# Kernel tuning notes

Hardware: AMD Instinct MI355X
Metric: run time of the kernel (lower is better)

Reference implementation:

```python
import jax, jax.numpy as jnp
import numpy as np

K = 1024          # num_embeddings
D = 256           # embedding_dim
COMMIT = 0.1      # commitment_cost
EPS = float(np.finfo(np.float32).eps)


def setup_inputs() -> dict:
    key = jax.random.key(0)
    k1, k2 = jax.random.split(key)
    X = jax.random.normal(k1, (16, 4096, D), dtype=jnp.float32)
    # matches nn.Embedding init: uniform(-1/K, 1/K)
    emb_weight = jax.random.uniform(k2, (K, D), dtype=jnp.float32,
                                    minval=-1.0 / K, maxval=1.0 / K)
    return {"X": X, "emb_weight": emb_weight}


def reference(X, emb_weight):
    B, N, Dm = X.shape
    Xf = X.reshape(-1, Dm)                                  # [BN, D]
    dist = (jnp.sum(Xf * Xf, axis=-1, keepdims=True)
            + jnp.sum(emb_weight * emb_weight, axis=-1)
            - 2.0 * Xf @ emb_weight.T)                      # [BN, K]
    idx = jnp.argmin(dist, axis=-1)                         # [BN]
    # one-hot @ codebook == gather
    quantized = emb_weight[idx].reshape(X.shape)            # [B, N, D]
    # perplexity from one-hot mean == normalized counts
    counts = jnp.zeros((K,), dtype=X.dtype).at[idx].add(1.0)
    avg_probs = counts / Xf.shape[0]
    perplexity = jnp.exp(-jnp.sum(avg_probs * jnp.log(avg_probs + EPS)))
    # vq loss (learnable codebook branch)
    sg = jax.lax.stop_gradient
    e_latent = jnp.mean((sg(quantized) - X) ** 2)
    q_latent = jnp.mean((quantized - sg(X)) ** 2)
    loss_vq = q_latent + COMMIT * e_latent
    # straight-through estimator
    quantized_st = X + sg(quantized - X)
    encoding_indices = idx.reshape(B, N)
    return quantized_st, encoding_indices, perplexity, loss_vq
```

## Files before the change

### kernel.cpp

```cpp
#include <hip/hip_runtime.h>
#include <math.h>

#define ROWS 65536
#define DIM  256
#define KC   1024
#define NQ   (ROWS * DIM)


__device__ __forceinline__ float half_sq_sum(const float* __restrict__ a) {
    float4 u0 = *(const float4*)(a);
    float4 u1 = *(const float4*)(a + 4);
    float r0 = __fmul_rn(u0.x, u0.x);
    float r1 = __fmul_rn(u0.y, u0.y);
    float r2 = __fmul_rn(u0.z, u0.z);
    float r3 = __fmul_rn(u0.w, u0.w);
    float r4 = __fmul_rn(u1.x, u1.x);
    float r5 = __fmul_rn(u1.y, u1.y);
    float r6 = __fmul_rn(u1.z, u1.z);
    float r7 = __fmul_rn(u1.w, u1.w);
    for (int i = 8; i < 128; i += 8) {
        float4 v0 = *(const float4*)(a + i);
        float4 v1 = *(const float4*)(a + i + 4);
        r0 = __fadd_rn(r0, __fmul_rn(v0.x, v0.x));
        r1 = __fadd_rn(r1, __fmul_rn(v0.y, v0.y));
        r2 = __fadd_rn(r2, __fmul_rn(v0.z, v0.z));
        r3 = __fadd_rn(r3, __fmul_rn(v0.w, v0.w));
        r4 = __fadd_rn(r4, __fmul_rn(v1.x, v1.x));
        r5 = __fadd_rn(r5, __fmul_rn(v1.y, v1.y));
        r6 = __fadd_rn(r6, __fmul_rn(v1.z, v1.z));
        r7 = __fadd_rn(r7, __fmul_rn(v1.w, v1.w));
    }
    float s01 = __fadd_rn(r0, r1);
    float s23 = __fadd_rn(r2, r3);
    float s45 = __fadd_rn(r4, r5);
    float s67 = __fadd_rn(r6, r7);
    return __fadd_rn(__fadd_rn(s01, s23), __fadd_rn(s45, s67));
}

__device__ __forceinline__ float sq_sum_numpy(const float* __restrict__ p) {
    float h0 = half_sq_sum(p);
    float h1 = half_sq_sum(p + 128);
    return __fadd_rn(h0, h1);
}

__global__ __launch_bounds__(256) void k_prepB(const float* __restrict__ E,
                                               float* __restrict__ B32) {
    int j = blockIdx.x * 256 + threadIdx.x;
    if (j >= KC) return;
    B32[j] = sq_sum_numpy(E + (size_t)j * DIM);
}

#define TM 128
#define TN 128
#define TD 32
#define BUFF 4096
#define BSTR 8192

__global__ __launch_bounds__(256, 2) void k_pass1(
    const float* __restrict__ X, const float* __restrict__ E,
    const float* __restrict__ B32, int* __restrict__ idx32)
{
    __shared__ __align__(16) float sm[2 * BSTR];

    const int tid = threadIdx.x;
    const int tx  = tid & 15;
    const int ty  = tid >> 4;
    const int rowbase = blockIdx.x * TM;

    float4 xv0, xv1, xv2, xv3, ev0, ev1, ev2, ev3;

#define LOADR(cbn, dcn)                                                         \
    do {                                                                        \
        int fi_, r_, d4_;                                                       \
        fi_ = tid;       r_ = fi_ >> 3; d4_ = (fi_ & 7) << 2;                   \
        xv0 = *(const float4*)(X + (size_t)(rowbase + r_) * DIM + (dcn) + d4_); \
        ev0 = *(const float4*)(E + (size_t)((cbn) + r_) * DIM + (dcn) + d4_);   \
        fi_ = tid + 256; r_ = fi_ >> 3; d4_ = (fi_ & 7) << 2;                   \
        xv1 = *(const float4*)(X + (size_t)(rowbase + r_) * DIM + (dcn) + d4_); \
        ev1 = *(const float4*)(E + (size_t)((cbn) + r_) * DIM + (dcn) + d4_);   \
        fi_ = tid + 512; r_ = fi_ >> 3; d4_ = (fi_ & 7) << 2;                   \
        xv2 = *(const float4*)(X + (size_t)(rowbase + r_) * DIM + (dcn) + d4_); \
        ev2 = *(const float4*)(E + (size_t)((cbn) + r_) * DIM + (dcn) + d4_);   \
        fi_ = tid + 768; r_ = fi_ >> 3; d4_ = (fi_ & 7) << 2;                   \
        xv3 = *(const float4*)(X + (size_t)(rowbase + r_) * DIM + (dcn) + d4_); \
        ev3 = *(const float4*)(E + (size_t)((cbn) + r_) * DIM + (dcn) + d4_);   \
    } while (0)

#define WRITE1(Xs_, Es_, v_, e_, fif_)                                          \
    do {                                                                        \
        int r_ = (fif_) >> 3, d4_ = ((fif_) & 7) << 2;                          \
        int off_ = d4_ * 128 + ((((r_) >> 2) ^ (d4_ >> 2)) << 2) + ((r_) & 3);  \
        (Xs_)[off_]       = v_.x; (Xs_)[off_ + 128] = v_.y;                     \
        (Xs_)[off_ + 256] = v_.z; (Xs_)[off_ + 384] = v_.w;                     \
        (Es_)[off_]       = e_.x; (Es_)[off_ + 128] = e_.y;                     \
        (Es_)[off_ + 256] = e_.z; (Es_)[off_ + 384] = e_.w;                     \
    } while (0)

#define WRITEB(b)                                                               \
    do {                                                                        \
        float* Xs_ = sm + (b) * BSTR;                                           \
        float* Es_ = Xs_ + BUFF;                                                \
        WRITE1(Xs_, Es_, xv0, ev0, tid);                                        \
        WRITE1(Xs_, Es_, xv1, ev1, tid + 256);                                  \
        WRITE1(Xs_, Es_, xv2, ev2, tid + 512);                                  \
        WRITE1(Xs_, Es_, xv3, ev3, tid + 768);                                  \
    } while (0)

    LOADR(0, 0);

    {
        int r = tid >> 1, h = tid & 1;
        sm[(r << 1) + h] = half_sq_sum(X + (size_t)(rowbase + r) * DIM + (h << 7));
    }
    __syncthreads();
    float a8[8];
#pragma unroll
    for (int i = 0; i < 8; ++i)
        a8[i] = __fadd_rn(sm[(ty * 8 + i) * 2], sm[(ty * 8 + i) * 2 + 1]);
    __syncthreads();
    WRITEB(0);

    float v1[8]; int i1[8];
#pragma unroll
    for (int i = 0; i < 8; ++i) { v1[i] = 3.0e38f; i1[i] = 0; }

    int cur = 0;
    for (int cb8 = 0; cb8 < 8; ++cb8) {
        const int cbase = cb8 * TN;
        float4 bq0 = *(const float4*)(B32 + cbase + (tx << 2));
        float4 bq1 = *(const float4*)(B32 + cbase + 64 + (tx << 2));

        float acc[8][8];
#pragma unroll
        for (int i = 0; i < 8; ++i)
#pragma unroll
            for (int j = 0; j < 8; ++j) acc[i][j] = 0.0f;

        for (int dc8 = 0; dc8 < 8; ++dc8) {
            const int s = cb8 * 8 + dc8;
            __syncthreads();
            if (s < 63) {
                const int sn = s + 1;
                LOADR((sn >> 3) * TN, (sn & 7) * TD);
            }
            {
                const float* Xc = sm + cur * BSTR;
                const float* Ec = Xc + BUFF;
#pragma unroll 2
                for (int dq = 0; dq < 8; ++dq) {
                    const float* xp0 = Xc + dq * 512 + ((((ty << 1)    ) ^ dq) << 2);
                    const float* xp1 = Xc + dq * 512 + ((((ty << 1) | 1) ^ dq) << 2);
                    const float* ep0 = Ec + dq * 512 + ((tx ^ dq) << 2);
#pragma unroll
                    for (int ddi = 0; ddi < 4; ++ddi) {
                        float4 t0 = *(const float4*)(xp0 + ddi * 128);
                        float4 t1 = *(const float4*)(xp1 + ddi * 128);
                        float4 u0 = *(const float4*)(ep0 + ddi * 128);
                        float4 u1 = *(const float4*)(ep0 + ddi * 128 + 64);
                        float xr[8] = {t0.x, t0.y, t0.z, t0.w, t1.x, t1.y, t1.z, t1.w};
                        float er[8] = {u0.x, u0.y, u0.z, u0.w, u1.x, u1.y, u1.z, u1.w};
#pragma unroll
                        for (int i = 0; i < 8; ++i)
#pragma unroll
                            for (int j = 0; j < 8; ++j)
                                acc[i][j] = fmaf(xr[i], er[j], acc[i][j]);
                    }
                }
            }
            if (s < 63) WRITEB(cur ^ 1);
            cur ^= 1;
        }

        float bvv[8] = {bq0.x, bq0.y, bq0.z, bq0.w, bq1.x, bq1.y, bq1.z, bq1.w};
#pragma unroll
        for (int j = 0; j < 8; ++j) {
            const int c = cbase + ((j < 4) ? ((tx << 2) + j)
                                           : (64 + (tx << 2) + (j - 4)));
#pragma unroll
            for (int i = 0; i < 8; ++i) {
                float Cv  = __fmul_rn(2.0f, acc[i][j]);
                float t1v = __fadd_rn(a8[i], bvv[j]);
                float dv  = __fsub_rn(t1v, Cv);
                if (dv < v1[i]) { v1[i] = dv; i1[i] = c; }
            }
        }
    }

    __syncthreads();
    float* Mv = sm;
    int*   Mi = (int*)(sm + 2048);
#pragma unroll
    for (int i = 0; i < 8; ++i) {
        int r = ty * 8 + i;
        Mv[r * 16 + tx] = v1[i];
        Mi[r * 16 + tx] = i1[i];
    }
    __syncthreads();
    if (tid < TM) {
        int r = tid;
        float bv = Mv[r * 16];
        int   bi = Mi[r * 16];
        for (int t = 1; t < 16; ++t) {
            float av = Mv[r * 16 + t];
            int   ai = Mi[r * 16 + t];
            if (av < bv || (av == bv && ai < bi)) { bv = av; bi = ai; }
        }
        idx32[rowbase + r] = bi;
    }
#undef LOADR
#undef WRITE1
#undef WRITEB
}

__global__ __launch_bounds__(256) void k_out(
    const float* __restrict__ X, const float* __restrict__ E,
    const int* __restrict__ idx32, float* __restrict__ out0,
    double* __restrict__ lossacc)
{
    const int NF4 = NQ / 4;
    double s = 0.0;
    for (int g = blockIdx.x * blockDim.x + threadIdx.x; g < NF4;
         g += gridDim.x * blockDim.x) {
        int row = g >> 6;
        int d4  = g & 63;
        int j = idx32[row];
        float4 q = *(const float4*)(E + (size_t)j * DIM + d4 * 4);
        float4 x = *(const float4*)(X + (size_t)g * 4);
        *(float4*)(out0 + (size_t)g * 4) = q;
        double dx;
        dx = (double)q.x - (double)x.x; s = fma(dx, dx, s);
        dx = (double)q.y - (double)x.y; s = fma(dx, dx, s);
        dx = (double)q.z - (double)x.z; s = fma(dx, dx, s);
        dx = (double)q.w - (double)x.w; s = fma(dx, dx, s);
    }
#pragma unroll
    for (int off = 32; off > 0; off >>= 1) s += __shfl_down(s, off, 64);
    __shared__ double wsum[4];
    int lane = threadIdx.x & 63, wv = threadIdx.x >> 6;
    if (lane == 0) wsum[wv] = s;
    __syncthreads();
    if (threadIdx.x == 0) {
        double t = wsum[0] + wsum[1] + wsum[2] + wsum[3];
        atomicAdd(lossacc, t);
    }
}

__global__ __launch_bounds__(256) void k_idxout(
    const int* __restrict__ idx32, float* __restrict__ out1,
    int* __restrict__ counts)
{
    __shared__ int h[KC];
    for (int i = threadIdx.x; i < KC; i += 256) h[i] = 0;
    __syncthreads();
    int r = blockIdx.x * 256 + threadIdx.x;
    int j = idx32[r];
    out1[r] = (float)j;
    atomicAdd(&h[j], 1);
    __syncthreads();
    for (int i = threadIdx.x; i < KC; i += 256)
        if (h[i]) atomicAdd(&counts[i], h[i]);
}

__global__ void k_fin(const int* __restrict__ counts,
                      const double* __restrict__ lossacc,
                      float* __restrict__ out_pl)
{
    __shared__ double sh[256];
    double s = 0.0;
    for (int i = threadIdx.x; i < KC; i += 256) {
        double p = (double)counts[i] / 65536.0;
        s += p * log(p + 1.1920928955078125e-07);
    }
    sh[threadIdx.x] = s;
    __syncthreads();
    for (int off = 128; off > 0; off >>= 1) {
        if (threadIdx.x < off) sh[threadIdx.x] += sh[threadIdx.x + off];
        __syncthreads();
    }
    if (threadIdx.x == 0) {
        out_pl[0] = (float)exp(-sh[0]);
        out_pl[1] = (float)((*lossacc / (double)NQ) * 1.1);
    }
}

extern "C" void kernel_launch(void* const* d_in, const int* in_sizes, int n_in,
                              void* d_out, int out_size, void* d_ws, size_t ws_size,
                              hipStream_t stream) {
    const float* X = (const float*)d_in[0];
    const float* E = (const float*)d_in[1];
    float* out = (float*)d_out;
    char* ws = (char*)d_ws;

    double* lossacc = (double*)(ws + 0);
    int*    counts  = (int*)(ws + 16);
    float*  B32     = (float*)(ws + 4224);
    int*    idx32   = (int*)(ws + 270464);

    hipMemsetAsync(d_ws, 0, 4224, stream);

    hipLaunchKernelGGL(k_prepB, dim3(4),         dim3(256), 0, stream, E, B32);
    hipLaunchKernelGGL(k_pass1, dim3(ROWS / TM), dim3(256), 0, stream,
                       X, E, B32, idx32);
    hipLaunchKernelGGL(k_out,   dim3(2048),      dim3(256), 0, stream,
                       X, E, idx32, out, lossacc);
    hipLaunchKernelGGL(k_idxout, dim3(256),      dim3(256), 0, stream,
                       idx32, out + NQ, counts);
    hipLaunchKernelGGL(k_fin,   dim3(1),         dim3(256), 0, stream,
                       counts, lossacc, out + NQ + 65536);
}
```

Measured before the change: 571.1 us.

## Fuse gather, loss and histogram into distance kernel; halve depth tile for occupancy

```diff
diff --git a/kernel.cpp b/kernel.cpp
--- a/kernel.cpp
+++ b/kernel.cpp
@@ -52,44 +52,41 @@
 
 #define TM 128
 #define TN 128
-#define TD 32
-#define BUFF 4096
-#define BSTR 8192
-
-__global__ __launch_bounds__(256, 2) void k_pass1(
+#define TD 16
+#define BUFF 2048
+#define BSTR 4096
+
+__global__ __launch_bounds__(256, 4) void k_pass1(
     const float* __restrict__ X, const float* __restrict__ E,
-    const float* __restrict__ B32, int* __restrict__ idx32)
+    const float* __restrict__ B32, float* __restrict__ out0,
+    float* __restrict__ out1, int* __restrict__ counts,
+    double* __restrict__ lossacc)
 {
-    __shared__ __align__(16) float sm[2 * BSTR];
+    __shared__ __align__(16) float sm[2 * BSTR + 128];
+    float* asq = sm + 2 * BSTR;
 
     const int tid = threadIdx.x;
     const int tx  = tid & 15;
     const int ty  = tid >> 4;
     const int rowbase = blockIdx.x * TM;
 
-    float4 xv0, xv1, xv2, xv3, ev0, ev1, ev2, ev3;
+    float4 xv0, xv1, ev0, ev1;
 
 #define LOADR(cbn, dcn)                                                         \
     do {                                                                        \
         int fi_, r_, d4_;                                                       \
-        fi_ = tid;       r_ = fi_ >> 3; d4_ = (fi_ & 7) << 2;                   \
+        fi_ = tid;       r_ = fi_ >> 2; d4_ = (fi_ & 3) << 2;                   \
         xv0 = *(const float4*)(X + (size_t)(rowbase + r_) * DIM + (dcn) + d4_); \
         ev0 = *(const float4*)(E + (size_t)((cbn) + r_) * DIM + (dcn) + d4_);   \
-        fi_ = tid + 256; r_ = fi_ >> 3; d4_ = (fi_ & 7) << 2;                   \
+        fi_ = tid + 256; r_ = fi_ >> 2; d4_ = (fi_ & 3) << 2;                   \
         xv1 = *(const float4*)(X + (size_t)(rowbase + r_) * DIM + (dcn) + d4_); \
         ev1 = *(const float4*)(E + (size_t)((cbn) + r_) * DIM + (dcn) + d4_);   \
-        fi_ = tid + 512; r_ = fi_ >> 3; d4_ = (fi_ & 7) << 2;                   \
-        xv2 = *(const float4*)(X + (size_t)(rowbase + r_) * DIM + (dcn) + d4_); \
-        ev2 = *(const float4*)(E + (size_t)((cbn) + r_) * DIM + (dcn) + d4_);   \
-        fi_ = tid + 768; r_ = fi_ >> 3; d4_ = (fi_ & 7) << 2;                   \
-        xv3 = *(const float4*)(X + (size_t)(rowbase + r_) * DIM + (dcn) + d4_); \
-        ev3 = *(const float4*)(E + (size_t)((cbn) + r_) * DIM + (dcn) + d4_);   \
     } while (0)
 
 #define WRITE1(Xs_, Es_, v_, e_, fif_)                                          \
     do {                                                                        \
-        int r_ = (fif_) >> 3, d4_ = ((fif_) & 7) << 2;                          \
-        int off_ = d4_ * 128 + ((((r_) >> 2) ^ (d4_ >> 2)) << 2) + ((r_) & 3);  \
+        int r_ = (fif_) >> 2, d4_ = ((fif_) & 3) << 2;                          \
+        int off_ = d4_ * 128 + ((((r_) >> 2) ^ ((d4_ >> 2) << 1)) << 2) + ((r_) & 3); \
         (Xs_)[off_]       = v_.x; (Xs_)[off_ + 128] = v_.y;                     \
         (Xs_)[off_ + 256] = v_.z; (Xs_)[off_ + 384] = v_.w;                     \
         (Es_)[off_]       = e_.x; (Es_)[off_ + 128] = e_.y;                     \
@@ -102,8 +99,6 @@
         float* Es_ = Xs_ + BUFF;                                                \
         WRITE1(Xs_, Es_, xv0, ev0, tid);                                        \
         WRITE1(Xs_, Es_, xv1, ev1, tid + 256);                                  \
-        WRITE1(Xs_, Es_, xv2, ev2, tid + 512);                                  \
-        WRITE1(Xs_, Es_, xv3, ev3, tid + 768);                                  \
     } while (0)
 
     LOADR(0, 0);
@@ -113,10 +108,7 @@
         sm[(r << 1) + h] = half_sq_sum(X + (size_t)(rowbase + r) * DIM + (h << 7));
     }
     __syncthreads();
-    float a8[8];
-#pragma unroll
-    for (int i = 0; i < 8; ++i)
-        a8[i] = __fadd_rn(sm[(ty * 8 + i) * 2], sm[(ty * 8 + i) * 2 + 1]);
+    if (tid < TM) asq[tid] = __fadd_rn(sm[tid << 1], sm[(tid << 1) + 1]);
     __syncthreads();
     WRITEB(0);
 
@@ -127,8 +119,6 @@
     int cur = 0;
     for (int cb8 = 0; cb8 < 8; ++cb8) {
         const int cbase = cb8 * TN;
-        float4 bq0 = *(const float4*)(B32 + cbase + (tx << 2));
-        float4 bq1 = *(const float4*)(B32 + cbase + 64 + (tx << 2));
 
         float acc[8][8];
 #pragma unroll
@@ -136,27 +126,28 @@
 #pragma unroll
             for (int j = 0; j < 8; ++j) acc[i][j] = 0.0f;
 
-        for (int dc8 = 0; dc8 < 8; ++dc8) {
-            const int s = cb8 * 8 + dc8;
+        for (int dcc = 0; dcc < 16; ++dcc) {
+            const int s = cb8 * 16 + dcc;
             __syncthreads();
-            if (s < 63) {
+            if (s < 127) {
                 const int sn = s + 1;
-                LOADR((sn >> 3) * TN, (sn & 7) * TD);
+                LOADR((sn >> 4) * TN, (sn & 15) * TD);
             }
             {
                 const float* Xc = sm + cur * BSTR;
                 const float* Ec = Xc + BUFF;
 #pragma unroll 2
-                for (int dq = 0; dq < 8; ++dq) {
-                    const float* xp0 = Xc + dq * 512 + ((((ty << 1)    ) ^ dq) << 2);
-                    const float* xp1 = Xc + dq * 512 + ((((ty << 1) | 1) ^ dq) << 2);
-                    const float* ep0 = Ec + dq * 512 + ((tx ^ dq) << 2);
-#pragma unroll
-                    for (int ddi = 0; ddi < 4; ++ddi) {
-                        float4 t0 = *(const float4*)(xp0 + ddi * 128);
-                        float4 t1 = *(const float4*)(xp1 + ddi * 128);
-                        float4 u0 = *(const float4*)(ep0 + ddi * 128);
-                        float4 u1 = *(const float4*)(ep0 + ddi * 128 + 64);
+                for (int q = 0; q < 4; ++q) {
+                    const int m = q << 1;
+                    const float* xp0 = Xc + q * 512 + (((2 * ty)     ^ m) << 2);
+                    const float* xp1 = Xc + q * 512 + (((2 * ty + 1) ^ m) << 2);
+                    const float* ep0 = Ec + q * 512 + ((tx ^ m) << 2);
+#pragma unroll
+                    for (int di = 0; di < 4; ++di) {
+                        float4 t0 = *(const float4*)(xp0 + di * 128);
+                        float4 t1 = *(const float4*)(xp1 + di * 128);
+                        float4 u0 = *(const float4*)(ep0 + di * 128);
+                        float4 u1 = *(const float4*)(ep0 + di * 128 + 64);
                         float xr[8] = {t0.x, t0.y, t0.z, t0.w, t1.x, t1.y, t1.z, t1.w};
                         float er[8] = {u0.x, u0.y, u0.z, u0.w, u1.x, u1.y, u1.z, u1.w};
 #pragma unroll
@@ -167,10 +158,12 @@
                     }
                 }
             }
-            if (s < 63) WRITEB(cur ^ 1);
+            if (s < 127) WRITEB(cur ^ 1);
             cur ^= 1;
         }
 
+        float4 bq0 = *(const float4*)(B32 + cbase + (tx << 2));
+        float4 bq1 = *(const float4*)(B32 + cbase + 64 + (tx << 2));
         float bvv[8] = {bq0.x, bq0.y, bq0.z, bq0.w, bq1.x, bq1.y, bq1.z, bq1.w};
 #pragma unroll
         for (int j = 0; j < 8; ++j) {
@@ -179,7 +172,7 @@
 #pragma unroll
             for (int i = 0; i < 8; ++i) {
                 float Cv  = __fmul_rn(2.0f, acc[i][j]);
-                float t1v = __fadd_rn(a8[i], bvv[j]);
+                float t1v = __fadd_rn(asq[ty * 8 + i], bvv[j]);
                 float dv  = __fsub_rn(t1v, Cv);
                 if (dv < v1[i]) { v1[i] = dv; i1[i] = c; }
             }
@@ -187,8 +180,9 @@
     }
 
     __syncthreads();
-    float* Mv = sm;
-    int*   Mi = (int*)(sm + 2048);
+    float* Mv  = sm;
+    int*   Mi  = (int*)(sm + 2048);
+    int*   sIdx = (int*)(sm + 4096);
 #pragma unroll
     for (int i = 0; i < 8; ++i) {
         int r = ty * 8 + i;
@@ -205,28 +199,23 @@
             int   ai = Mi[r * 16 + t];
             if (av < bv || (av == bv && ai < bi)) { bv = av; bi = ai; }
         }
-        idx32[rowbase + r] = bi;
-    }
-#undef LOADR
-#undef WRITE1
-#undef WRITEB
-}
-
-__global__ __launch_bounds__(256) void k_out(
-    const float* __restrict__ X, const float* __restrict__ E,
-    const int* __restrict__ idx32, float* __restrict__ out0,
-    double* __restrict__ lossacc)
-{
-    const int NF4 = NQ / 4;
+        sIdx[r] = bi;
+        out1[rowbase + r] = (float)bi;
+        atomicAdd(&counts[bi], 1);
+    }
+    __syncthreads();
+
+    const size_t base = (size_t)rowbase * DIM;
     double s = 0.0;
-    for (int g = blockIdx.x * blockDim.x + threadIdx.x; g < NF4;
-         g += gridDim.x * blockDim.x) {
-        int row = g >> 6;
-        int d4  = g & 63;
-        int j = idx32[row];
+#pragma unroll 4
+    for (int g = 0; g < 32; ++g) {
+        int fi  = tid + g * 256;
+        int row = fi >> 6;
+        int d4  = fi & 63;
+        int j = sIdx[row];
         float4 q = *(const float4*)(E + (size_t)j * DIM + d4 * 4);
-        float4 x = *(const float4*)(X + (size_t)g * 4);
-        *(float4*)(out0 + (size_t)g * 4) = q;
+        float4 x = *(const float4*)(X + base + (size_t)fi * 4);
+        *(float4*)(out0 + base + (size_t)fi * 4) = q;
         double dx;
         dx = (double)q.x - (double)x.x; s = fma(dx, dx, s);
         dx = (double)q.y - (double)x.y; s = fma(dx, dx, s);
@@ -235,30 +224,17 @@
     }
 #pragma unroll
     for (int off = 32; off > 0; off >>= 1) s += __shfl_down(s, off, 64);
-    __shared__ double wsum[4];
-    int lane = threadIdx.x & 63, wv = threadIdx.x >> 6;
+    double* wsum = (double*)(sm + 4352);
+    int lane = tid & 63, wv = tid >> 6;
     if (lane == 0) wsum[wv] = s;
     __syncthreads();
-    if (threadIdx.x == 0) {
+    if (tid == 0) {
         double t = wsum[0] + wsum[1] + wsum[2] + wsum[3];
         atomicAdd(lossacc, t);
     }
-}
-
-__global__ __launch_bounds__(256) void k_idxout(
-    const int* __restrict__ idx32, float* __restrict__ out1,
-    int* __restrict__ counts)
-{
-    __shared__ int h[KC];
-    for (int i = threadIdx.x; i < KC; i += 256) h[i] = 0;
-    __syncthreads();
-    int r = blockIdx.x * 256 + threadIdx.x;
-    int j = idx32[r];
-    out1[r] = (float)j;
-    atomicAdd(&h[j], 1);
-    __syncthreads();
-    for (int i = threadIdx.x; i < KC; i += 256)
-        if (h[i]) atomicAdd(&counts[i], h[i]);
+#undef LOADR
+#undef WRITE1
+#undef WRITEB
 }
 
 __global__ void k_fin(const int* __restrict__ counts,
@@ -294,17 +270,12 @@
     double* lossacc = (double*)(ws + 0);
     int*    counts  = (int*)(ws + 16);
     float*  B32     = (float*)(ws + 4224);
-    int*    idx32   = (int*)(ws + 270464);
 
     hipMemsetAsync(d_ws, 0, 4224, stream);
 
     hipLaunchKernelGGL(k_prepB, dim3(4),         dim3(256), 0, stream, E, B32);
     hipLaunchKernelGGL(k_pass1, dim3(ROWS / TM), dim3(256), 0, stream,
-                       X, E, B32, idx32);
-    hipLaunchKernelGGL(k_out,   dim3(2048),      dim3(256), 0, stream,
-                       X, E, idx32, out, lossacc);
-    hipLaunchKernelGGL(k_idxout, dim3(256),      dim3(256), 0, stream,
-                       idx32, out + NQ, counts);
+                       X, E, B32, out, out + NQ, counts, lossacc);
     hipLaunchKernelGGL(k_fin,   dim3(1),         dim3(256), 0, stream,
                        counts, lossacc, out + NQ + 65536);
 }
```

Result: slower. 904.7 us (+58.4%).

## Fuse gather, loss and histogram into distance kernel; use packed FMA

Applied to the files above, without the earlier changes.

```diff
diff --git a/kernel.cpp b/kernel.cpp
--- a/kernel.cpp
+++ b/kernel.cpp
@@ -5,6 +5,8 @@
 #define DIM  256
 #define KC   1024
 #define NQ   (ROWS * DIM)
+
+typedef float f2 __attribute__((ext_vector_type(2)));
 
 
 __device__ __forceinline__ float half_sq_sum(const float* __restrict__ a) {
@@ -58,7 +60,9 @@
 
 __global__ __launch_bounds__(256, 2) void k_pass1(
     const float* __restrict__ X, const float* __restrict__ E,
-    const float* __restrict__ B32, int* __restrict__ idx32)
+    const float* __restrict__ B32, float* __restrict__ out0,
+    float* __restrict__ out1, int* __restrict__ counts,
+    double* __restrict__ lossacc)
 {
     __shared__ __align__(16) float sm[2 * BSTR];
 
@@ -127,14 +131,12 @@
     int cur = 0;
     for (int cb8 = 0; cb8 < 8; ++cb8) {
         const int cbase = cb8 * TN;
-        float4 bq0 = *(const float4*)(B32 + cbase + (tx << 2));
-        float4 bq1 = *(const float4*)(B32 + cbase + 64 + (tx << 2));
-
-        float acc[8][8];
+
+        f2 acc[8][4];
 #pragma unroll
         for (int i = 0; i < 8; ++i)
 #pragma unroll
-            for (int j = 0; j < 8; ++j) acc[i][j] = 0.0f;
+            for (int j = 0; j < 4; ++j) acc[i][j] = (f2){0.0f, 0.0f};
 
         for (int dc8 = 0; dc8 < 8; ++dc8) {
             const int s = cb8 * 8 + dc8;
@@ -157,13 +159,21 @@
                         float4 t1 = *(const float4*)(xp1 + ddi * 128);
                         float4 u0 = *(const float4*)(ep0 + ddi * 128);
                         float4 u1 = *(const float4*)(ep0 + ddi * 128 + 64);
-                        float xr[8] = {t0.x, t0.y, t0.z, t0.w, t1.x, t1.y, t1.z, t1.w};
-                        float er[8] = {u0.x, u0.y, u0.z, u0.w, u1.x, u1.y, u1.z, u1.w};
-#pragma unroll
-                        for (int i = 0; i < 8; ++i)
-#pragma unroll
-                            for (int j = 0; j < 8; ++j)
-                                acc[i][j] = fmaf(xr[i], er[j], acc[i][j]);
+                        f2 e0 = {u0.x, u0.y};
+                        f2 e1 = {u0.z, u0.w};
+                        f2 e2 = {u1.x, u1.y};
+                        f2 e3 = {u1.z, u1.w};
+#define ROWF(i_, xs_)                                                           \
+                        {                                                       \
+                            f2 xp_ = {xs_, xs_};                                \
+                            acc[i_][0] = __builtin_elementwise_fma(xp_, e0, acc[i_][0]); \
+                            acc[i_][1] = __builtin_elementwise_fma(xp_, e1, acc[i_][1]); \
+                            acc[i_][2] = __builtin_elementwise_fma(xp_, e2, acc[i_][2]); \
+                            acc[i_][3] = __builtin_elementwise_fma(xp_, e3, acc[i_][3]); \
+                        }
+                        ROWF(0, t0.x) ROWF(1, t0.y) ROWF(2, t0.z) ROWF(3, t0.w)
+                        ROWF(4, t1.x) ROWF(5, t1.y) ROWF(6, t1.z) ROWF(7, t1.w)
+#undef ROWF
                     }
                 }
             }
@@ -171,6 +181,8 @@
             cur ^= 1;
         }
 
+        float4 bq0 = *(const float4*)(B32 + cbase + (tx << 2));
+        float4 bq1 = *(const float4*)(B32 + cbase + 64 + (tx << 2));
         float bvv[8] = {bq0.x, bq0.y, bq0.z, bq0.w, bq1.x, bq1.y, bq1.z, bq1.w};
 #pragma unroll
         for (int j = 0; j < 8; ++j) {
@@ -178,7 +190,8 @@
                                            : (64 + (tx << 2) + (j - 4)));
 #pragma unroll
             for (int i = 0; i < 8; ++i) {
-                float Cv  = __fmul_rn(2.0f, acc[i][j]);
+                float av  = acc[i][j >> 1][j & 1];
+                float Cv  = __fmul_rn(2.0f, av);
                 float t1v = __fadd_rn(a8[i], bvv[j]);
                 float dv  = __fsub_rn(t1v, Cv);
                 if (dv < v1[i]) { v1[i] = dv; i1[i] = c; }
@@ -187,8 +200,10 @@
     }
 
     __syncthreads();
-    float* Mv = sm;
-    int*   Mi = (int*)(sm + 2048);
+    float* Mv   = sm;
+    int*   Mi   = (int*)(sm + 2048);
+    int*   sIdx = (int*)(sm + 4096);
+    double* wsum = (double*)(sm + 4224);
 #pragma unroll
     for (int i = 0; i < 8; ++i) {
         int r = ty * 8 + i;
@@ -205,28 +220,23 @@
             int   ai = Mi[r * 16 + t];
             if (av < bv || (av == bv && ai < bi)) { bv = av; bi = ai; }
         }
-        idx32[rowbase + r] = bi;
-    }
-#undef LOADR
-#undef WRITE1
-#undef WRITEB
-}
-
-__global__ __launch_bounds__(256) void k_out(
-    const float* __restrict__ X, const float* __restrict__ E,
-    const int* __restrict__ idx32, float* __restrict__ out0,
-    double* __restrict__ lossacc)
-{
-    const int NF4 = NQ / 4;
+        sIdx[r] = bi;
+        out1[rowbase + r] = (float)bi;
+        atomicAdd(&counts[bi], 1);
+    }
+    __syncthreads();
+
+    const size_t base = (size_t)rowbase * DIM;
     double s = 0.0;
-    for (int g = blockIdx.x * blockDim.x + threadIdx.x; g < NF4;
-         g += gridDim.x * blockDim.x) {
-        int row = g >> 6;
-        int d4  = g & 63;
-        int j = idx32[row];
+#pragma unroll 4
+    for (int g = 0; g < 32; ++g) {
+        int fi  = tid + g * 256;
+        int row = fi >> 6;
+        int d4  = fi & 63;
+        int j = sIdx[row];
         float4 q = *(const float4*)(E + (size_t)j * DIM + d4 * 4);
-        float4 x = *(const float4*)(X + (size_t)g * 4);
-        *(float4*)(out0 + (size_t)g * 4) = q;
+        float4 x = *(const float4*)(X + base + (size_t)fi * 4);
+        *(float4*)(out0 + base + (size_t)fi * 4) = q;
         double dx;
         dx = (double)q.x - (double)x.x; s = fma(dx, dx, s);
         dx = (double)q.y - (double)x.y; s = fma(dx, dx, s);
@@ -235,30 +245,16 @@
     }
 #pragma unroll
     for (int off = 32; off > 0; off >>= 1) s += __shfl_down(s, off, 64);
-    __shared__ double wsum[4];
-    int lane = threadIdx.x & 63, wv = threadIdx.x >> 6;
+    int lane = tid & 63, wv = tid >> 6;
     if (lane == 0) wsum[wv] = s;
     __syncthreads();
-    if (threadIdx.x == 0) {
+    if (tid == 0) {
         double t = wsum[0] + wsum[1] + wsum[2] + wsum[3];
         atomicAdd(lossacc, t);
     }
-}
-
-__global__ __launch_bounds__(256) void k_idxout(
-    const int* __restrict__ idx32, float* __restrict__ out1,
-    int* __restrict__ counts)
-{
-    __shared__ int h[KC];
-    for (int i = threadIdx.x; i < KC; i += 256) h[i] = 0;
-    __syncthreads();
-    int r = blockIdx.x * 256 + threadIdx.x;
-    int j = idx32[r];
-    out1[r] = (float)j;
-    atomicAdd(&h[j], 1);
-    __syncthreads();
-    for (int i = threadIdx.x; i < KC; i += 256)
-        if (h[i]) atomicAdd(&counts[i], h[i]);
+#undef LOADR
+#undef WRITE1
+#undef WRITEB
 }
 
 __global__ void k_fin(const int* __restrict__ counts,
@@ -294,17 +290,12 @@
     double* lossacc = (double*)(ws + 0);
     int*    counts  = (int*)(ws + 16);
     float*  B32     = (float*)(ws + 4224);
-    int*    idx32   = (int*)(ws + 270464);
 
     hipMemsetAsync(d_ws, 0, 4224, stream);
 
     hipLaunchKernelGGL(k_prepB, dim3(4),         dim3(256), 0, stream, E, B32);
     hipLaunchKernelGGL(k_pass1, dim3(ROWS / TM), dim3(256), 0, stream,
-                       X, E, B32, idx32);
-    hipLaunchKernelGGL(k_out,   dim3(2048),      dim3(256), 0, stream,
-                       X, E, idx32, out, lossacc);
-    hipLaunchKernelGGL(k_idxout, dim3(256),      dim3(256), 0, stream,
-                       idx32, out + NQ, counts);
+                       X, E, B32, out, out + NQ, counts, lossacc);
     hipLaunchKernelGGL(k_fin,   dim3(1),         dim3(256), 0, stream,
                        counts, lossacc, out + NQ + 65536);
 }
```

Measured after the change: 532.0 us. -6.8%, faster.
